# Performance work log

Hardware: AMD Instinct MI355X
Metric: run time of the kernel (lower is better)

Reference implementation:

```python
import jax, jax.numpy as jnp
import numpy as np

EMBED = 1024
HEADS = 16


def setup_inputs() -> dict:
    key = jax.random.key(0)
    ks = jax.random.split(key, 12)
    s = 1.0 / np.sqrt(EMBED)
    return {
        "x": jax.random.normal(ks[0], (1, EMBED, 128, 128), jnp.float32),
        "masks": jax.random.normal(ks[1], (200, 128, 128), jnp.float32),
        "Wq": jax.random.normal(ks[2], (EMBED, EMBED), jnp.float32) * s,
        "bq": jax.random.normal(ks[3], (EMBED,), jnp.float32) * 0.02,
        "Wk": jax.random.normal(ks[4], (EMBED, EMBED), jnp.float32) * s,
        "bk": jax.random.normal(ks[5], (EMBED,), jnp.float32) * 0.02,
        "Wv": jax.random.normal(ks[6], (EMBED, EMBED), jnp.float32) * s,
        "bv": jax.random.normal(ks[7], (EMBED,), jnp.float32) * 0.02,
        "Wc": jax.random.normal(ks[8], (EMBED, EMBED), jnp.float32) * s,
        "bc": jax.random.normal(ks[9], (EMBED,), jnp.float32) * 0.02,
    }


def reference(x, masks, Wq, bq, Wk, bk, Wv, bv, Wc, bc):
    # x: [1, C, H, W], masks: [Q, H, W]  (way4 branch, batch must be 1)
    N, C, H, W = x.shape
    Q = masks.shape[0]
    HW = H * W
    nh = HEADS
    hd = C // nh

    xs = x.reshape(C, HW).T                      # [HW, C] pixel tokens
    m = jax.nn.sigmoid(masks).reshape(Q, HW).T   # [HW, Q]

    # mask-weighted mean pooling (avoid materializing [HW, Q, C])
    w = jnp.sum(m, axis=0)                       # [Q]
    mean = jnp.einsum('lq,lc->qc', m, xs) / (w[:, None] + 0.001)  # [Q, C]

    seq = jnp.concatenate([mean, xs], axis=0)    # [L, C], L = Q + HW
    L = Q + HW

    q = (mean @ Wq.T + bq).reshape(Q, nh, hd) * (hd ** -0.5)
    k = (seq @ Wk.T + bk).reshape(L, nh, hd)
    v = (seq @ Wv.T + bv).reshape(L, nh, hd)

    # bool attn mask [Q, L]: True = disallowed
    qq = ~jnp.eye(Q, dtype=bool)                 # only self among pooled queries
    qp = (m.T <= 0.9)                            # pixels with sigmoid <= 0.9 masked
    attn_mask = jnp.concatenate([qq, qp], axis=1)  # [Q, L]

    scores = jnp.einsum('qhd,lhd->hql', q, k)    # [nh, Q, L]
    scores = jnp.where(attn_mask[None], -jnp.inf, scores)
    probs = jax.nn.softmax(scores, axis=-1)
    ctx = jnp.einsum('hql,lhd->qhd', probs, v).reshape(Q, C)
    out = ctx @ Wc.T + bc                        # [Q, out_dim]
    return out.reshape(Q, 1, -1)                 # match torch [Q, batch=1, out_dim]
```

## Files before the change

kernel.cpp:

```cpp
#include <hip/hip_runtime.h>
#include <math.h>

#define HW_  16384
#define Q_   200
#define C_   1024
#define L_   16584
#define NH_  16
#define HD_  64
#define CAP  512
#define KSPLIT 8
#define KCH  (HW_ / KSPLIT)
#define ASPLIT 4
#define SK   8

typedef __attribute__((ext_vector_type(8))) __bf16 bf16x8;
typedef __attribute__((ext_vector_type(8))) unsigned short u16x8;
typedef __attribute__((ext_vector_type(4))) unsigned short u16x4;
typedef __attribute__((ext_vector_type(4))) float f32x4;

__device__ inline unsigned short f2bf(float f) {
  unsigned int u = __float_as_uint(f);
  u += 0x7fff + ((u >> 16) & 1);
  return (unsigned short)(u >> 16);
}
__device__ inline float bf2f(unsigned short u) {
  return __uint_as_float((unsigned int)u << 16);
}


__global__ __launch_bounds__(256) void k_sigmoid_w(const float* __restrict__ masks,
                                                   float* __restrict__ msig,
                                                   unsigned short* __restrict__ msigbf,
                                                   float* __restrict__ w) {
  int q = blockIdx.x;
  int tid = threadIdx.x;
  unsigned short* obf = msigbf + (size_t)q * HW_;
  if (q >= Q_) {
    u16x4 z = {0, 0, 0, 0};
    for (int i = tid; i < HW_ / 4; i += 256) *(u16x4*)&obf[i * 4] = z;
    return;
  }
  const float4* mrow4 = (const float4*)(masks + (size_t)q * HW_);
  float4* orow4 = (float4*)(msig + (size_t)q * HW_);
  float s = 0.f;
  for (int i = tid; i < HW_ / 4; i += 256) {
    float4 v = mrow4[i];
    float4 sg;
    sg.x = 1.f / (1.f + expf(-v.x));
    sg.y = 1.f / (1.f + expf(-v.y));
    sg.z = 1.f / (1.f + expf(-v.z));
    sg.w = 1.f / (1.f + expf(-v.w));
    orow4[i] = sg;
    u16x4 o = {f2bf(sg.x), f2bf(sg.y), f2bf(sg.z), f2bf(sg.w)};
    *(u16x4*)&obf[i * 4] = o;
    s += sg.x + sg.y + sg.z + sg.w;
  }
  __shared__ float red[256];
  red[tid] = s;
  __syncthreads();
  for (int off = 128; off > 0; off >>= 1) {
    if (tid < off) red[tid] += red[tid + off];
    __syncthreads();
  }
  if (tid == 0) w[q] = red[0];
}

__global__ __launch_bounds__(256) void k_compact(const float* __restrict__ msig,
                                                 int* __restrict__ cnt,
                                                 int* __restrict__ idxg) {
  int q = blockIdx.x;
  int tid = threadIdx.x;
  const float* mrow = msig + (size_t)q * HW_;
  const int CHUNK = HW_ / 256;
  int base = tid * CHUNK;
  int my = 0;
  for (int j = 0; j < CHUNK; j++) my += (mrow[base + j] > 0.9f) ? 1 : 0;
  __shared__ int sc[256];
  sc[tid] = my;
  __syncthreads();
  for (int off = 1; off < 256; off <<= 1) {
    int v = sc[tid];
    int add = (tid >= off) ? sc[tid - off] : 0;
    __syncthreads();
    sc[tid] = v + add;
    __syncthreads();
  }
  int excl = sc[tid] - my;
  int total = sc[255];
  int* orow = idxg + (size_t)q * CAP;
  int off = 1 + excl;
  for (int j = 0; j < CHUNK; j++) {
    if (mrow[base + j] > 0.9f) {
      if (off < CAP) orow[off] = Q_ + base + j;
      off++;
    }
  }
  if (tid == 0) {
    orow[0] = q;
    int c = 1 + total;
    cnt[q] = c < CAP ? c : CAP;
  }
}

__global__ __launch_bounds__(256) void k_xcast(const float* __restrict__ x,
                                               unsigned short* __restrict__ xbf,
                                               unsigned short* __restrict__ seqbf) {
  __shared__ float t[32][33];
  int l0 = blockIdx.x * 32, c0 = blockIdx.y * 32;
  int tx = threadIdx.x, ty = threadIdx.y;
  #pragma unroll
  for (int i = 0; i < 32; i += 8) {
    float v = x[(size_t)(c0 + ty + i) * HW_ + l0 + tx];
    t[ty + i][tx] = v;
    xbf[(size_t)(c0 + ty + i) * HW_ + l0 + tx] = f2bf(v);
  }
  __syncthreads();
  #pragma unroll
  for (int i = 0; i < 32; i += 8)
    seqbf[(size_t)(Q_ + l0 + ty + i) * C_ + c0 + tx] = f2bf(t[tx][ty + i]);
}

__global__ __launch_bounds__(256) void k_cast4(const float* __restrict__ s0,
                                               const float* __restrict__ s1,
                                               const float* __restrict__ s2,
                                               const float* __restrict__ s3,
                                               unsigned short* __restrict__ d0,
                                               unsigned short* __restrict__ d1,
                                               unsigned short* __restrict__ d2,
                                               unsigned short* __restrict__ d3) {
  const float* src = (blockIdx.y == 0) ? s0 : (blockIdx.y == 1) ? s1
                     : (blockIdx.y == 2) ? s2 : s3;
  unsigned short* dst = (blockIdx.y == 0) ? d0 : (blockIdx.y == 1) ? d1
                        : (blockIdx.y == 2) ? d2 : d3;
  int i = (blockIdx.x * 256 + threadIdx.x) * 4;
  float4 v = *(const float4*)&src[i];
  u16x4 o = {f2bf(v.x), f2bf(v.y), f2bf(v.z), f2bf(v.w)};
  *(u16x4*)&dst[i] = o;
}

#define GBM 128
#define GBN 128
#define GBK 32

__global__ __launch_bounds__(512) void k_gemm_kv(const unsigned short* __restrict__ A,
                                                 const unsigned short* __restrict__ Bk,
                                                 const unsigned short* __restrict__ Bv,
                                                 const float* __restrict__ bk,
                                                 const float* __restrict__ bv,
                                                 unsigned short* __restrict__ Ko,
                                                 unsigned short* __restrict__ Vo,
                                                 int M, int K) {
  __shared__ __attribute__((aligned(16))) unsigned short smem[3][3 * GBM * GBK];
  int w = blockIdx.x;
  int nbm = gridDim.x >> 3;
  int t = (w >> 3) + (w & 7) * nbm;
  int bm = (t >> 3) * GBM;
  int bn = (t & 7) * GBN;
  int tid = threadIdx.x;
  int wid = tid >> 6, lane = tid & 63;
  int w2 = wid & 3;
  int wr = w2 >> 1, wc = w2 & 1;
  int fq = lane >> 4, fr = lane & 15;
  int srow = lane >> 2;
  int scol = (((lane & 3) ^ ((lane >> 3) & 3)) * 8);
  int sslot = (fq ^ ((fr >> 1) & 3)) * 8;
  int boff = (wid < 4) ? GBM * GBK : 2 * GBM * GBK;

  auto stage = [&](int buf, int k0) {
    #pragma unroll
    for (int i = 0; i < 3; i++) {
      int ci = wid * 3 + i;
      const unsigned short* src;
      if (ci < 8) {
        int gA = bm + ci * 16 + srow; if (gA > M - 1) gA = M - 1;
        src = A + (size_t)gA * K + k0 + scol;
      } else if (ci < 16) {
        src = Bk + (size_t)(bn + (ci - 8) * 16 + srow) * K + k0 + scol;
      } else {
        src = Bv + (size_t)(bn + (ci - 16) * 16 + srow) * K + k0 + scol;
      }
      __builtin_amdgcn_global_load_lds(
          (const __attribute__((address_space(1))) void*)src,
          (__attribute__((address_space(3))) void*)((char*)&smem[buf][0] + ci * 1024),
          16, 0, 0);
    }
  };

  f32x4 acc[4][4] = {};
  const int NT = K / GBK;
  stage(0, 0);
  stage(1, GBK);
  for (int it = 0; it < NT; it++) {
    int cur = it % 3;
    if (it + 2 < NT) {
      stage((it + 2) % 3, (it + 2) * GBK);
      asm volatile("s_waitcnt vmcnt(6)" ::: "memory");
    } else if (it + 1 < NT) {
      asm volatile("s_waitcnt vmcnt(3)" ::: "memory");
    } else {
      asm volatile("s_waitcnt vmcnt(0)" ::: "memory");
    }
    __builtin_amdgcn_s_barrier();
    asm volatile("" ::: "memory");
    const unsigned short (*As)[GBK]  = (const unsigned short (*)[GBK])(&smem[cur][0]);
    const unsigned short (*Bts)[GBK] = (const unsigned short (*)[GBK])(&smem[cur][0] + boff);
    bf16x8 af[4], bfr[4];
    #pragma unroll
    for (int mi = 0; mi < 4; mi++)
      af[mi] = *(const bf16x8*)&As[wr * 64 + mi * 16 + fr][sslot];
    #pragma unroll
    for (int ni = 0; ni < 4; ni++)
      bfr[ni] = *(const bf16x8*)&Bts[wc * 64 + ni * 16 + fr][sslot];
    #pragma unroll
    for (int mi = 0; mi < 4; mi++)
      #pragma unroll
      for (int ni = 0; ni < 4; ni++)
        acc[mi][ni] = __builtin_amdgcn_mfma_f32_16x16x32_bf16(bfr[ni], af[mi], acc[mi][ni], 0, 0, 0);
    asm volatile("" ::: "memory");
    __builtin_amdgcn_s_barrier();
    asm volatile("" ::: "memory");
  }
  const float* bias = (wid < 4) ? bk : bv;
  unsigned short* Cout = (wid < 4) ? Ko : Vo;
  #pragma unroll
  for (int mi = 0; mi < 4; mi++) {
    int m = bm + wr * 64 + mi * 16 + fr;
    if (m >= M) continue;
    #pragma unroll
    for (int ni = 0; ni < 4; ni++) {
      int n0 = bn + wc * 64 + ni * 16 + fq * 4;
      float4 b4 = *(const float4*)&bias[n0];
      u16x4 o = {f2bf(acc[mi][ni][0] + b4.x), f2bf(acc[mi][ni][1] + b4.y),
                 f2bf(acc[mi][ni][2] + b4.z), f2bf(acc[mi][ni][3] + b4.w)};
      *(u16x4*)&Cout[(size_t)m * C_ + n0] = o;
    }
  }
}

__global__ __launch_bounds__(256) void k_gemm_meank(const unsigned short* __restrict__ A,
                                                    const unsigned short* __restrict__ B,
                                                    float* __restrict__ partial) {
  __shared__ __attribute__((aligned(16))) unsigned short As[2][GBM][GBK];
  __shared__ __attribute__((aligned(16))) unsigned short Bs[2][GBN][GBK];
  int bm = blockIdx.y * GBM, bn = blockIdx.x * GBN;
  int kc = blockIdx.z;
  int tid = threadIdx.x;
  int wid = tid >> 6, lane = tid & 63;
  int wr = wid >> 1, wc = wid & 1;
  int fq = lane >> 4, fr = lane & 15;
  int srow = lane >> 2;
  int scol = (((lane & 3) ^ ((lane >> 3) & 3)) * 8);
  int sslot = (fq ^ ((fr >> 1) & 3)) * 8;

  auto stage = [&](int buf, int k0) {
    #pragma unroll
    for (int i = 0; i < 2; i++) {
      int r = wid * 32 + i * 16 + srow;
      __builtin_amdgcn_global_load_lds(
          (const __attribute__((address_space(1))) void*)(A + (size_t)(bm + r) * HW_ + k0 + scol),
          (__attribute__((address_space(3))) void*)((char*)&As[buf][0][0] + (wid * 2 + i) * 1024),
          16, 0, 0);
      __builtin_amdgcn_global_load_lds(
          (const __attribute__((address_space(1))) void*)(B + (size_t)(bn + r) * HW_ + k0 + scol),
          (__attribute__((address_space(3))) void*)((char*)&Bs[buf][0][0] + (wid * 2 + i) * 1024),
          16, 0, 0);
    }
  };

  f32x4 acc[4][4] = {};
  int kbeg = kc * KCH;
  const int NT = KCH / GBK;
  stage(0, kbeg);
  __syncthreads();
  int cur = 0;
  for (int it = 0; it < NT; it++) {
    if (it + 1 < NT) stage(cur ^ 1, kbeg + (it + 1) * GBK);
    bf16x8 af[4], bfr[4];
    #pragma unroll
    for (int mi = 0; mi < 4; mi++)
      af[mi] = *(const bf16x8*)&As[cur][wr * 64 + mi * 16 + fr][sslot];
    #pragma unroll
    for (int ni = 0; ni < 4; ni++)
      bfr[ni] = *(const bf16x8*)&Bs[cur][wc * 64 + ni * 16 + fr][sslot];
    #pragma unroll
    for (int mi = 0; mi < 4; mi++)
      #pragma unroll
      for (int ni = 0; ni < 4; ni++)
        acc[mi][ni] = __builtin_amdgcn_mfma_f32_16x16x32_bf16(bfr[ni], af[mi], acc[mi][ni], 0, 0, 0);
    __syncthreads();
    cur ^= 1;
  }
  #pragma unroll
  for (int mi = 0; mi < 4; mi++) {
    int m = bm + wr * 64 + mi * 16 + fr;
    #pragma unroll
    for (int ni = 0; ni < 4; ni++) {
      int n0 = bn + wc * 64 + ni * 16 + fq * 4;
      *(f32x4*)&partial[((size_t)kc * 256 + m) * C_ + n0] = acc[mi][ni];
    }
  }
}

__global__ __launch_bounds__(256) void k_mean_reduce(const float* __restrict__ partial,
                                                     const float* __restrict__ w,
                                                     unsigned short* __restrict__ seqbf) {
  int m = blockIdx.x;
  float rs = 1.f / (w[m] + 0.001f);
  for (int n = threadIdx.x; n < C_; n += 256) {
    float s = 0.f;
    #pragma unroll
    for (int kc = 0; kc < KSPLIT; kc++)
      s += partial[((size_t)kc * 256 + m) * C_ + n];
    seqbf[(size_t)m * C_ + n] = f2bf(s * rs);
  }
}

__global__ __launch_bounds__(256) void k_gemm_splitk_bf(const unsigned short* __restrict__ A,
                                                        const unsigned short* __restrict__ B,
                                                        float* __restrict__ partial,
                                                        int M, int K) {
  __shared__ __attribute__((aligned(16))) unsigned short As[2][GBM][GBK];
  __shared__ __attribute__((aligned(16))) unsigned short Bs[2][GBN][GBK];
  int bm = blockIdx.y * GBM, bn = blockIdx.x * GBN;
  int kc = blockIdx.z;
  int kchunk = K / SK;
  int tid = threadIdx.x;
  int wid = tid >> 6, lane = tid & 63;
  int wr = wid >> 1, wc = wid & 1;
  int fq = lane >> 4, fr = lane & 15;
  int srow = lane >> 2;
  int scol = (((lane & 3) ^ ((lane >> 3) & 3)) * 8);
  int sslot = (fq ^ ((fr >> 1) & 3)) * 8;

  auto stage = [&](int buf, int k0) {
    #pragma unroll
    for (int i = 0; i < 2; i++) {
      int r = wid * 32 + i * 16 + srow;
      int gA = bm + r; if (gA > M - 1) gA = M - 1;
      __builtin_amdgcn_global_load_lds(
          (const __attribute__((address_space(1))) void*)(A + (size_t)gA * K + k0 + scol),
          (__attribute__((address_space(3))) void*)((char*)&As[buf][0][0] + (wid * 2 + i) * 1024),
          16, 0, 0);
      __builtin_amdgcn_global_load_lds(
          (const __attribute__((address_space(1))) void*)(B + (size_t)(bn + r) * K + k0 + scol),
          (__attribute__((address_space(3))) void*)((char*)&Bs[buf][0][0] + (wid * 2 + i) * 1024),
          16, 0, 0);
    }
  };

  f32x4 acc[4][4] = {};
  int kbeg = kc * kchunk;
  const int NT = kchunk / GBK;
  stage(0, kbeg);
  __syncthreads();
  int cur = 0;
  for (int it = 0; it < NT; it++) {
    if (it + 1 < NT) stage(cur ^ 1, kbeg + (it + 1) * GBK);
    bf16x8 af[4], bfr[4];
    #pragma unroll
    for (int mi = 0; mi < 4; mi++)
      af[mi] = *(const bf16x8*)&As[cur][wr * 64 + mi * 16 + fr][sslot];
    #pragma unroll
    for (int ni = 0; ni < 4; ni++)
      bfr[ni] = *(const bf16x8*)&Bs[cur][wc * 64 + ni * 16 + fr][sslot];
    #pragma unroll
    for (int mi = 0; mi < 4; mi++)
      #pragma unroll
      for (int ni = 0; ni < 4; ni++)
        acc[mi][ni] = __builtin_amdgcn_mfma_f32_16x16x32_bf16(bfr[ni], af[mi], acc[mi][ni], 0, 0, 0);
    __syncthreads();
    cur ^= 1;
  }
  #pragma unroll
  for (int mi = 0; mi < 4; mi++) {
    int m = bm + wr * 64 + mi * 16 + fr;
    #pragma unroll
    for (int ni = 0; ni < 4; ni++) {
      int n0 = bn + wc * 64 + ni * 16 + fq * 4;
      *(f32x4*)&partial[((size_t)kc * 256 + m) * C_ + n0] = acc[mi][ni];
    }
  }
}

__global__ __launch_bounds__(256) void k_splitk_reduce(const float* __restrict__ partial,
                                                       const float* __restrict__ bias,
                                                       float* __restrict__ outf) {
  int m = blockIdx.x;
  for (int n = threadIdx.x; n < C_; n += 256) {
    float s = 0.f;
    #pragma unroll
    for (int kc = 0; kc < SK; kc++)
      s += partial[((size_t)kc * 256 + m) * C_ + n];
    outf[(size_t)m * C_ + n] = s + bias[n];
  }
}

__global__ __launch_bounds__(256) void k_attn_split(const float* __restrict__ qb,
                                                    const unsigned short* __restrict__ kb,
                                                    const unsigned short* __restrict__ vb,
                                                    const int* __restrict__ cnt_g,
                                                    const int* __restrict__ idxg,
                                                    float* __restrict__ pmax,
                                                    float* __restrict__ psum,
                                                    float* __restrict__ pacc) {
  int q = blockIdx.x, h = blockIdx.y, sp = blockIdx.z;
  int tid = threadIdx.x;
  int lane = tid & 63, wid = tid >> 6;

  __shared__ float qs[64];
  __shared__ float sc[CAP / ASPLIT];
  __shared__ int   ls[CAP / ASPLIT];
  __shared__ float wred[4];
  __shared__ float accb[4][64];

  int cnt = cnt_g[q];
  int cq = (cnt + ASPLIT - 1) / ASPLIT;
  int beg = sp * cq;
  int end = beg + cq; if (end > cnt) end = cnt;
  int ns = end - beg; if (ns < 0) ns = 0;

  if (tid < 64) qs[tid] = qb[(size_t)q * C_ + h * HD_ + tid] * 0.125f;
  __syncthreads();

  if (tid < ns) {
    int l = idxg[(size_t)q * CAP + beg + tid];
    ls[tid] = l;
    const u16x8* kr = (const u16x8*)(kb + (size_t)l * C_ + h * HD_);
    float s = 0.f;
    #pragma unroll
    for (int v8 = 0; v8 < 8; v8++) {
      u16x8 kv = kr[v8];
      #pragma unroll
      for (int e = 0; e < 8; e++) s = fmaf(qs[v8 * 8 + e], bf2f(kv[e]), s);
    }
    sc[tid] = s;
  }
  __syncthreads();

  float lm = (tid < ns) ? sc[tid] : -INFINITY;
  #pragma unroll
  for (int off = 32; off; off >>= 1) lm = fmaxf(lm, __shfl_xor(lm, off));
  if (lane == 0) wred[wid] = lm;
  __syncthreads();
  float m4 = fmaxf(fmaxf(wred[0], wred[1]), fmaxf(wred[2], wred[3]));

  float e = 0.f;
  if (tid < ns) {
    e = expf(sc[tid] - m4);
    sc[tid] = e;
  }
  float lsum = e;
  #pragma unroll
  for (int off = 32; off; off >>= 1) lsum += __shfl_xor(lsum, off);
  __syncthreads();
  if (lane == 0) wred[wid] = lsum;
  __syncthreads();
  float S4 = wred[0] + wred[1] + wred[2] + wred[3];

  float acc = 0.f;
  for (int j = wid; j < ns; j += 4)
    acc = fmaf(sc[j], bf2f(vb[(size_t)ls[j] * C_ + h * HD_ + lane]), acc);
  accb[wid][lane] = acc;
  __syncthreads();

  int pidx = (q * NH_ + h) * ASPLIT + sp;
  if (tid < 64)
    pacc[(size_t)pidx * 64 + tid] =
        accb[0][tid] + accb[1][tid] + accb[2][tid] + accb[3][tid];
  if (tid == 0) {
    pmax[pidx] = (ns > 0) ? m4 : -INFINITY;
    psum[pidx] = S4;
  }
}

__global__ __launch_bounds__(64) void k_attn_merge(const float* __restrict__ pmax,
                                                   const float* __restrict__ psum,
                                                   const float* __restrict__ pacc,
                                                   unsigned short* __restrict__ ctxbf) {
  int q = blockIdx.x, h = blockIdx.y;
  int d = threadIdx.x;
  int base = (q * NH_ + h) * ASPLIT;
  float M = -INFINITY;
  #pragma unroll
  for (int s = 0; s < ASPLIT; s++) M = fmaxf(M, pmax[base + s]);
  float S = 0.f, a = 0.f;
  #pragma unroll
  for (int s = 0; s < ASPLIT; s++) {
    float wgt = expf(pmax[base + s] - M);
    S += psum[base + s] * wgt;
    a += pacc[(size_t)(base + s) * 64 + d] * wgt;
  }
  ctxbf[(size_t)q * C_ + h * HD_ + d] = f2bf(a / S);
}

extern "C" void kernel_launch(void* const* d_in, const int* in_sizes, int n_in,
                              void* d_out, int out_size, void* d_ws, size_t ws_size,
                              hipStream_t stream) {
  const float* x     = (const float*)d_in[0];
  const float* masks = (const float*)d_in[1];
  const float* Wq    = (const float*)d_in[2];
  const float* bq    = (const float*)d_in[3];
  const float* Wk    = (const float*)d_in[4];
  const float* bk    = (const float*)d_in[5];
  const float* Wv    = (const float*)d_in[6];
  const float* bv    = (const float*)d_in[7];
  const float* Wc    = (const float*)d_in[8];
  const float* bc    = (const float*)d_in[9];
  float* out = (float*)d_out;

  char* p = (char*)d_ws;
  auto alloc = [&](size_t bytes) {
    char* r = p;
    p += (bytes + 255) & ~(size_t)255;
    return r;
  };
  float* msig    = (float*)alloc((size_t)Q_ * HW_ * 4);
  float* w       = (float*)alloc(1024);
  float* qbuf    = (float*)alloc((size_t)Q_ * C_ * 4);
  float* partial = (float*)alloc((size_t)KSPLIT * 256 * C_ * 4);
  int*   cnt     = (int*)alloc(1024);
  int*   idxg    = (int*)alloc((size_t)Q_ * CAP * 4);
  float* pmax    = (float*)alloc((size_t)Q_ * NH_ * ASPLIT * 4);
  float* psum    = (float*)alloc((size_t)Q_ * NH_ * ASPLIT * 4);
  float* pacc    = (float*)alloc((size_t)Q_ * NH_ * ASPLIT * 64 * 4);
  unsigned short* msigbf = (unsigned short*)alloc((size_t)256 * HW_ * 2);
  unsigned short* xbf    = (unsigned short*)alloc((size_t)C_ * HW_ * 2);
  unsigned short* seqbf  = (unsigned short*)alloc((size_t)L_ * C_ * 2);
  unsigned short* wkbf   = (unsigned short*)alloc((size_t)C_ * C_ * 2);
  unsigned short* wvbf   = (unsigned short*)alloc((size_t)C_ * C_ * 2);
  unsigned short* wqbf   = (unsigned short*)alloc((size_t)C_ * C_ * 2);
  unsigned short* wcbf   = (unsigned short*)alloc((size_t)C_ * C_ * 2);
  unsigned short* ctxbf  = (unsigned short*)alloc((size_t)256 * C_ * 2);
  unsigned short* kbuf   = (unsigned short*)alloc((size_t)L_ * C_ * 2);
  unsigned short* vbuf   = (unsigned short*)alloc((size_t)L_ * C_ * 2);

  k_sigmoid_w<<<256, 256, 0, stream>>>(masks, msig, msigbf, w);
  k_compact<<<Q_, 256, 0, stream>>>(msig, cnt, idxg);
  k_xcast<<<dim3(HW_ / 32, C_ / 32), dim3(32, 8), 0, stream>>>(x, xbf, seqbf);
  k_cast4<<<dim3(C_ * C_ / 1024, 4), 256, 0, stream>>>(Wk, Wv, Wq, Wc,
                                                       wkbf, wvbf, wqbf, wcbf);
  k_gemm_meank<<<dim3(C_ / GBN, 2, KSPLIT), 256, 0, stream>>>(msigbf, xbf, partial);
  k_mean_reduce<<<Q_, 256, 0, stream>>>(partial, w, seqbf);
  k_gemm_splitk_bf<<<dim3(C_ / GBN, 2, SK), 256, 0, stream>>>(seqbf, wqbf, partial, Q_, C_);
  k_splitk_reduce<<<Q_, 256, 0, stream>>>(partial, bq, qbuf);
  k_gemm_kv<<<8 * ((L_ + GBM - 1) / GBM), 512, 0, stream>>>(
      seqbf, wkbf, wvbf, bk, bv, kbuf, vbuf, L_, C_);
  k_attn_split<<<dim3(Q_, NH_, ASPLIT), 256, 0, stream>>>(
      qbuf, kbuf, vbuf, cnt, idxg, pmax, psum, pacc);
  k_attn_merge<<<dim3(Q_, NH_), 64, 0, stream>>>(pmax, psum, pacc, ctxbf);
  k_gemm_splitk_bf<<<dim3(C_ / GBN, 2, SK), 256, 0, stream>>>(ctxbf, wcbf, partial, Q_, C_);
  k_splitk_reduce<<<Q_, 256, 0, stream>>>(partial, bc, out);
}
```

Measured before the change: 302.4 us.

## Fuse sigmoid with mask compaction and retile KV GEMM to 4 waves

Merges the sigmoid/weight-sum kernel with the compaction kernel. Each thread now processes a contiguous 64-element chunk and keeps a 64-bit mask of the sigmoid>0.9 hits, so the fp32 sigmoid buffer is never written and re-read. Separately, the fused K/V GEMM drops from 8 waves to 4 waves per block; each wave computes a 64x128 tile with twice the accumulators and issues twice as many LDS-load stages. The MFMA section is also bracketed with s_setprio. This raises register pressure per wave in exchange for more B-fragment reuse, with launch bounds (256,2) set to keep two blocks per CU.

```diff
diff --git a/kernel.cpp b/kernel.cpp
--- a/kernel.cpp
+++ b/kernel.cpp
@@ -28,10 +28,11 @@
 }
 
 
-__global__ __launch_bounds__(256) void k_sigmoid_w(const float* __restrict__ masks,
-                                                   float* __restrict__ msig,
-                                                   unsigned short* __restrict__ msigbf,
-                                                   float* __restrict__ w) {
+__global__ __launch_bounds__(256) void k_sig_compact(const float* __restrict__ masks,
+                                                     unsigned short* __restrict__ msigbf,
+                                                     float* __restrict__ w,
+                                                     int* __restrict__ cnt,
+                                                     int* __restrict__ idxg) {
   int q = blockIdx.x;
   int tid = threadIdx.x;
   unsigned short* obf = msigbf + (size_t)q * HW_;
@@ -40,44 +41,37 @@
     for (int i = tid; i < HW_ / 4; i += 256) *(u16x4*)&obf[i * 4] = z;
     return;
   }
-  const float4* mrow4 = (const float4*)(masks + (size_t)q * HW_);
-  float4* orow4 = (float4*)(msig + (size_t)q * HW_);
+  const float* mrow = masks + (size_t)q * HW_;
+  const int base = tid * 64;
+  unsigned long long bits = 0;
   float s = 0.f;
-  for (int i = tid; i < HW_ / 4; i += 256) {
-    float4 v = mrow4[i];
-    float4 sg;
-    sg.x = 1.f / (1.f + expf(-v.x));
-    sg.y = 1.f / (1.f + expf(-v.y));
-    sg.z = 1.f / (1.f + expf(-v.z));
-    sg.w = 1.f / (1.f + expf(-v.w));
-    orow4[i] = sg;
-    u16x4 o = {f2bf(sg.x), f2bf(sg.y), f2bf(sg.z), f2bf(sg.w)};
-    *(u16x4*)&obf[i * 4] = o;
-    s += sg.x + sg.y + sg.z + sg.w;
-  }
+  #pragma unroll
+  for (int j4 = 0; j4 < 16; j4++) {
+    float4 v = *(const float4*)&mrow[base + j4 * 4];
+    float sg0 = 1.f / (1.f + expf(-v.x));
+    float sg1 = 1.f / (1.f + expf(-v.y));
+    float sg2 = 1.f / (1.f + expf(-v.z));
+    float sg3 = 1.f / (1.f + expf(-v.w));
+    u16x4 o = {f2bf(sg0), f2bf(sg1), f2bf(sg2), f2bf(sg3)};
+    *(u16x4*)&obf[base + j4 * 4] = o;
+    s += sg0 + sg1 + sg2 + sg3;
+    if (sg0 > 0.9f) bits |= 1ull << (j4 * 4 + 0);
+    if (sg1 > 0.9f) bits |= 1ull << (j4 * 4 + 1);
+    if (sg2 > 0.9f) bits |= 1ull << (j4 * 4 + 2);
+    if (sg3 > 0.9f) bits |= 1ull << (j4 * 4 + 3);
+  }
+  int my = __popcll(bits);
+
   __shared__ float red[256];
+  __shared__ int sc[256];
   red[tid] = s;
+  sc[tid] = my;
   __syncthreads();
   for (int off = 128; off > 0; off >>= 1) {
     if (tid < off) red[tid] += red[tid + off];
     __syncthreads();
   }
   if (tid == 0) w[q] = red[0];
-}
-
-__global__ __launch_bounds__(256) void k_compact(const float* __restrict__ msig,
-                                                 int* __restrict__ cnt,
-                                                 int* __restrict__ idxg) {
-  int q = blockIdx.x;
-  int tid = threadIdx.x;
-  const float* mrow = msig + (size_t)q * HW_;
-  const int CHUNK = HW_ / 256;
-  int base = tid * CHUNK;
-  int my = 0;
-  for (int j = 0; j < CHUNK; j++) my += (mrow[base + j] > 0.9f) ? 1 : 0;
-  __shared__ int sc[256];
-  sc[tid] = my;
-  __syncthreads();
   for (int off = 1; off < 256; off <<= 1) {
     int v = sc[tid];
     int add = (tid >= off) ? sc[tid - off] : 0;
@@ -89,8 +83,8 @@
   int total = sc[255];
   int* orow = idxg + (size_t)q * CAP;
   int off = 1 + excl;
-  for (int j = 0; j < CHUNK; j++) {
-    if (mrow[base + j] > 0.9f) {
+  for (int j = 0; j < 64; j++) {
+    if ((bits >> j) & 1ull) {
       if (off < CAP) orow[off] = Q_ + base + j;
       off++;
     }
@@ -142,14 +136,14 @@
 #define GBN 128
 #define GBK 32
 
-__global__ __launch_bounds__(512) void k_gemm_kv(const unsigned short* __restrict__ A,
-                                                 const unsigned short* __restrict__ Bk,
-                                                 const unsigned short* __restrict__ Bv,
-                                                 const float* __restrict__ bk,
-                                                 const float* __restrict__ bv,
-                                                 unsigned short* __restrict__ Ko,
-                                                 unsigned short* __restrict__ Vo,
-                                                 int M, int K) {
+__global__ __launch_bounds__(256, 2) void k_gemm_kv(const unsigned short* __restrict__ A,
+                                                    const unsigned short* __restrict__ Bk,
+                                                    const unsigned short* __restrict__ Bv,
+                                                    const float* __restrict__ bk,
+                                                    const float* __restrict__ bv,
+                                                    unsigned short* __restrict__ Ko,
+                                                    unsigned short* __restrict__ Vo,
+                                                    int M, int K) {
   __shared__ __attribute__((aligned(16))) unsigned short smem[3][3 * GBM * GBK];
   int w = blockIdx.x;
   int nbm = gridDim.x >> 3;
@@ -158,18 +152,18 @@
   int bn = (t & 7) * GBN;
   int tid = threadIdx.x;
   int wid = tid >> 6, lane = tid & 63;
-  int w2 = wid & 3;
-  int wr = w2 >> 1, wc = w2 & 1;
+  int half = wid >> 1;
+  int whalf = wid & 1;
   int fq = lane >> 4, fr = lane & 15;
   int srow = lane >> 2;
   int scol = (((lane & 3) ^ ((lane >> 3) & 3)) * 8);
   int sslot = (fq ^ ((fr >> 1) & 3)) * 8;
-  int boff = (wid < 4) ? GBM * GBK : 2 * GBM * GBK;
+  int boff = (half == 0) ? GBM * GBK : 2 * GBM * GBK;
 
   auto stage = [&](int buf, int k0) {
     #pragma unroll
-    for (int i = 0; i < 3; i++) {
-      int ci = wid * 3 + i;
+    for (int i = 0; i < 6; i++) {
+      int ci = wid * 6 + i;
       const unsigned short* src;
       if (ci < 8) {
         int gA = bm + ci * 16 + srow; if (gA > M - 1) gA = M - 1;
@@ -186,7 +180,7 @@
     }
   };
 
-  f32x4 acc[4][4] = {};
+  f32x4 acc[4][8] = {};
   const int NT = K / GBK;
   stage(0, 0);
   stage(1, GBK);
@@ -194,9 +188,9 @@
     int cur = it % 3;
     if (it + 2 < NT) {
       stage((it + 2) % 3, (it + 2) * GBK);
+      asm volatile("s_waitcnt vmcnt(12)" ::: "memory");
+    } else if (it + 1 < NT) {
       asm volatile("s_waitcnt vmcnt(6)" ::: "memory");
-    } else if (it + 1 < NT) {
-      asm volatile("s_waitcnt vmcnt(3)" ::: "memory");
     } else {
       asm volatile("s_waitcnt vmcnt(0)" ::: "memory");
     }
@@ -204,31 +198,33 @@
     asm volatile("" ::: "memory");
     const unsigned short (*As)[GBK]  = (const unsigned short (*)[GBK])(&smem[cur][0]);
     const unsigned short (*Bts)[GBK] = (const unsigned short (*)[GBK])(&smem[cur][0] + boff);
-    bf16x8 af[4], bfr[4];
+    bf16x8 af[4], bfr[8];
     #pragma unroll
     for (int mi = 0; mi < 4; mi++)
-      af[mi] = *(const bf16x8*)&As[wr * 64 + mi * 16 + fr][sslot];
-    #pragma unroll
-    for (int ni = 0; ni < 4; ni++)
-      bfr[ni] = *(const bf16x8*)&Bts[wc * 64 + ni * 16 + fr][sslot];
+      af[mi] = *(const bf16x8*)&As[whalf * 64 + mi * 16 + fr][sslot];
+    #pragma unroll
+    for (int ni = 0; ni < 8; ni++)
+      bfr[ni] = *(const bf16x8*)&Bts[ni * 16 + fr][sslot];
+    __builtin_amdgcn_s_setprio(1);
     #pragma unroll
     for (int mi = 0; mi < 4; mi++)
       #pragma unroll
-      for (int ni = 0; ni < 4; ni++)
+      for (int ni = 0; ni < 8; ni++)
         acc[mi][ni] = __builtin_amdgcn_mfma_f32_16x16x32_bf16(bfr[ni], af[mi], acc[mi][ni], 0, 0, 0);
+    __builtin_amdgcn_s_setprio(0);
     asm volatile("" ::: "memory");
     __builtin_amdgcn_s_barrier();
     asm volatile("" ::: "memory");
   }
-  const float* bias = (wid < 4) ? bk : bv;
-  unsigned short* Cout = (wid < 4) ? Ko : Vo;
+  const float* bias = (half == 0) ? bk : bv;
+  unsigned short* Cout = (half == 0) ? Ko : Vo;
   #pragma unroll
   for (int mi = 0; mi < 4; mi++) {
-    int m = bm + wr * 64 + mi * 16 + fr;
+    int m = bm + whalf * 64 + mi * 16 + fr;
     if (m >= M) continue;
     #pragma unroll
-    for (int ni = 0; ni < 4; ni++) {
-      int n0 = bn + wc * 64 + ni * 16 + fq * 4;
+    for (int ni = 0; ni < 8; ni++) {
+      int n0 = bn + ni * 16 + fq * 4;
       float4 b4 = *(const float4*)&bias[n0];
       u16x4 o = {f2bf(acc[mi][ni][0] + b4.x), f2bf(acc[mi][ni][1] + b4.y),
                  f2bf(acc[mi][ni][2] + b4.z), f2bf(acc[mi][ni][3] + b4.w)};
@@ -514,7 +510,6 @@
     p += (bytes + 255) & ~(size_t)255;
     return r;
   };
-  float* msig    = (float*)alloc((size_t)Q_ * HW_ * 4);
   float* w       = (float*)alloc(1024);
   float* qbuf    = (float*)alloc((size_t)Q_ * C_ * 4);
   float* partial = (float*)alloc((size_t)KSPLIT * 256 * C_ * 4);
@@ -534,8 +529,7 @@
   unsigned short* kbuf   = (unsigned short*)alloc((size_t)L_ * C_ * 2);
   unsigned short* vbuf   = (unsigned short*)alloc((size_t)L_ * C_ * 2);
 
-  k_sigmoid_w<<<256, 256, 0, stream>>>(masks, msig, msigbf, w);
-  k_compact<<<Q_, 256, 0, stream>>>(msig, cnt, idxg);
+  k_sig_compact<<<256, 256, 0, stream>>>(masks, msigbf, w, cnt, idxg);
   k_xcast<<<dim3(HW_ / 32, C_ / 32), dim3(32, 8), 0, stream>>>(x, xbf, seqbf);
   k_cast4<<<dim3(C_ * C_ / 1024, 4), 256, 0, stream>>>(Wk, Wv, Wq, Wc,
                                                        wkbf, wvbf, wqbf, wcbf);
@@ -543,7 +537,7 @@
   k_mean_reduce<<<Q_, 256, 0, stream>>>(partial, w, seqbf);
   k_gemm_splitk_bf<<<dim3(C_ / GBN, 2, SK), 256, 0, stream>>>(seqbf, wqbf, partial, Q_, C_);
   k_splitk_reduce<<<Q_, 256, 0, stream>>>(partial, bq, qbuf);
-  k_gemm_kv<<<8 * ((L_ + GBM - 1) / GBM), 512, 0, stream>>>(
+  k_gemm_kv<<<8 * ((L_ + GBM - 1) / GBM), 256, 0, stream>>>(
       seqbf, wkbf, wvbf, bk, bv, kbuf, vbuf, L_, C_);
   k_attn_split<<<dim3(Q_, NH_, ASPLIT), 256, 0, stream>>>(
       qbuf, kbuf, vbuf, cnt, idxg, pmax, psum, pacc);
```

Result: faster. 286.2 us (-5.3%).
